# Performance work log

Hardware: AMD Instinct MI355X
Metric: run time of the kernel (lower is better)

The kernel has to match this reference:

```python
import jax, jax.numpy as jnp
import numpy as np

# ---- module hyperparameters (from init_kwargs) ----
DIM = 16        # Hilbert-space dimension (density matrix is DIM x DIM)
BATCH = 32      # number of initial states evolved in parallel
K_LIND = 4      # number of Lindblad collapse operators
N_TS = 512      # number of Euler integration steps
N_CTRLS = 4     # number of control channels
N_PARAMS = 16   # B-spline control points per channel
DEGREE = 3      # cubic B-splines
T_TOTAL = 1.0
DT = T_TOTAL / N_TS


def _bspline_basis_matrix(t, knots, degree):
    """Cox-de Boor recursion, vectorized over all basis functions.
    t: (n_ts,), knots: (n_knots,). Returns (n_ts, n_knots-1-degree)."""
    k = knots
    # degree-0: indicator of half-open knot spans -> (n_ts, n_knots-1)
    B = ((k[None, :-1] <= t[:, None]) & (t[:, None] < k[None, 1:])).astype(t.dtype)
    for d in range(1, degree + 1):
        left_den = k[d:-1] - k[:-(d + 1)]
        right_den = k[d + 1:] - k[1:-d]
        left = jnp.where(left_den > 0,
                         (t[:, None] - k[None, :-(d + 1)]) / jnp.where(left_den > 0, left_den, 1.0) * B[:, :-1],
                         0.0)
        right = jnp.where(right_den > 0,
                          (k[None, d + 1:] - t[:, None]) / jnp.where(right_den > 0, right_den, 1.0) * B[:, 1:],
                          0.0)
        B = left + right
    return B  # (n_ts, n_knots - 1 - degree) == (n_ts, N_PARAMS)


def setup_inputs() -> dict:
    key = jax.random.key(0)
    ks = jax.random.split(key, 10)
    f32 = jnp.float32
    params = 0.5 * jax.random.normal(ks[0], (N_PARAMS, N_CTRLS), f32)
    H0_re = jax.random.normal(ks[1], (DIM, DIM), f32)
    H0_im = jax.random.normal(ks[2], (DIM, DIM), f32)
    Hc_re = jax.random.normal(ks[3], (N_CTRLS, DIM, DIM), f32)
    Hc_im = jax.random.normal(ks[4], (N_CTRLS, DIM, DIM), f32)
    L_re = 0.3 * jax.random.normal(ks[5], (K_LIND, DIM, DIM), f32)
    L_im = 0.3 * jax.random.normal(ks[6], (K_LIND, DIM, DIM), f32)
    # valid density matrices: rho0 = A A^dag / tr(A A^dag)
    A = (jax.random.normal(ks[7], (BATCH, DIM, DIM), f32)
         + 1j * jax.random.normal(ks[8], (BATCH, DIM, DIM), f32)).astype(jnp.complex64)
    rho0 = jnp.einsum('bij,bkj->bik', A, A.conj())
    tr = jnp.trace(rho0, axis1=-2, axis2=-1).real[:, None, None]
    rho0 = rho0 / tr.astype(jnp.complex64)
    return {
        'params': params,
        'H0_re': H0_re, 'H0_im': H0_im,
        'Hc_re': Hc_re, 'Hc_im': Hc_im,
        'L_re': L_re, 'L_im': L_im,
        'rho0_re': jnp.real(rho0).astype(f32),
        'rho0_im': jnp.imag(rho0).astype(f32),
    }


def reference(params, H0_re, H0_im, Hc_re, Hc_im, L_re, L_im, rho0_re, rho0_im):
    c64 = jnp.complex64
    # Hermitize Hamiltonians
    H0 = (H0_re + 1j * H0_im).astype(c64)
    H0 = 0.5 * (H0 + H0.conj().T)
    Hc = (Hc_re + 1j * Hc_im).astype(c64)
    Hc = 0.5 * (Hc + jnp.conj(jnp.swapaxes(Hc, -1, -2)))
    L = (L_re + 1j * L_im).astype(c64)              # (K, d, d)
    LdL = jnp.einsum('kji,kjl->il', L.conj(), L)    # sum_k L^dag L  (d, d)
    rho0 = (rho0_re + 1j * rho0_im).astype(c64)     # (B, d, d)

    # B-spline control pulses (clamped knot vector, as in evaluate_bspline_batch)
    t = jnp.arange(N_TS, dtype=jnp.float32) * DT
    knots = jnp.concatenate([
        jnp.zeros(DEGREE, jnp.float32),
        jnp.linspace(0.0, T_TOTAL, N_PARAMS - DEGREE + 1).astype(jnp.float32),
        T_TOTAL * jnp.ones(DEGREE, jnp.float32),
    ])
    basis = _bspline_basis_matrix(t, knots, DEGREE)  # (n_ts, n_params)
    u = basis @ params                               # (n_ts, n_ctrls)

    def step(rho, u_t):
        H = H0 + jnp.einsum('c,cij->ij', u_t.astype(c64), Hc)
        jump = jnp.einsum('kij,bjl,kml->bim', L, rho, L.conj())
        drho = (-1j) * (H @ rho - rho @ H) + jump - 0.5 * (LdL @ rho + rho @ LdL)
        rho_new = rho + DT * drho
        pops = jnp.real(jnp.diagonal(rho_new, axis1=-2, axis2=-1)).astype(jnp.float32)
        return rho_new, pops

    _, pops = jax.lax.scan(step, rho0, u)
    return pops  # (n_ts, batch, dim) real populations
```

## Files before the change

kernel.cpp:

```cpp
#include <hip/hip_runtime.h>
#include <hip/hip_bf16.h>

#define DIM    16
#define BATCH  32
#define KL     4
#define NTS    512
#define NC     4
#define NPAR   16
#define DTF    (1.0f/512.0f)
#define BST    40

using short8  = __attribute__((ext_vector_type(8))) short;
using short4v = __attribute__((ext_vector_type(4))) short;
using f32x4   = __attribute__((ext_vector_type(4))) float;

__device__ __forceinline__ float b2f(__hip_bfloat16 x) { return __bfloat162float(x); }

__device__ __forceinline__ float ldval(const void* p, int idx, bool isf32) {
  return isf32 ? ((const float*)p)[idx]
               : __bfloat162float(((const __hip_bfloat16*)p)[idx]);
}
__device__ __forceinline__ unsigned short f2bf(float x) {
  unsigned u = __float_as_uint(x);
  unsigned r = u + 0x7FFFu + ((u >> 16) & 1u);
  return (unsigned short)(r >> 16);
}
__device__ __forceinline__ float bf2f(unsigned short h) {
  return __uint_as_float(((unsigned)h) << 16);
}
__device__ __forceinline__ void split2(float v, unsigned short& h, unsigned short& l) {
  unsigned u = __float_as_uint(v);
  h = (unsigned short)(u >> 16);
  float r = v - __uint_as_float(u & 0xFFFF0000u);
  l = (unsigned short)(__float_as_uint(r) >> 16);
}
__device__ __forceinline__ short8 ldfrag(const unsigned short* p) {
  return *(const short8*)p;
}
__device__ __forceinline__ short8 negbf8(short8 a) {
  union { short8 s; unsigned u[4]; } v; v.s = a;
  #pragma unroll
  for (int q = 0; q < 4; ++q) v.u[q] ^= 0x80008000u;
  return v.s;
}
__device__ __forceinline__ f32x4 mm3(short8 Ah, short8 Al, short8 Bh, short8 Bl, f32x4 acc) {
  acc = __builtin_amdgcn_mfma_f32_16x16x32_bf16(Ah, Bh, acc, 0, 0, 0);
  acc = __builtin_amdgcn_mfma_f32_16x16x32_bf16(Al, Bh, acc, 0, 0, 0);
  acc = __builtin_amdgcn_mfma_f32_16x16x32_bf16(Ah, Bl, acc, 0, 0, 0);
  return acc;
}
__device__ __forceinline__ f32x4 mm3b(short8 Ah, short8 Al, short8 Bh, short8 Bl, f32x4 acc) {
  acc = __builtin_amdgcn_mfma_f32_16x16x32_bf16(Ah, Bh, acc, 0, 0, 0);
  acc = __builtin_amdgcn_mfma_f32_16x16x32_bf16(Ah, Bl, acc, 0, 0, 0);
  acc = __builtin_amdgcn_mfma_f32_16x16x32_bf16(Al, Bh, acc, 0, 0, 0);
  return acc;
}
__device__ __forceinline__ void pack4(f32x4 v, short4v& hi, short4v& lo) {
  union { short4v s; unsigned d[2]; } H, L;
  unsigned u0 = __float_as_uint(v[0]), u1 = __float_as_uint(v[1]);
  unsigned u2 = __float_as_uint(v[2]), u3 = __float_as_uint(v[3]);
  H.d[0] = __builtin_amdgcn_perm(u1, u0, 0x07060302u);
  H.d[1] = __builtin_amdgcn_perm(u3, u2, 0x07060302u);
  float r0 = v[0] - __uint_as_float(u0 & 0xFFFF0000u);
  float r1 = v[1] - __uint_as_float(u1 & 0xFFFF0000u);
  float r2 = v[2] - __uint_as_float(u2 & 0xFFFF0000u);
  float r3 = v[3] - __uint_as_float(u3 & 0xFFFF0000u);
  L.d[0] = __builtin_amdgcn_perm(__float_as_uint(r1), __float_as_uint(r0), 0x07060302u);
  L.d[1] = __builtin_amdgcn_perm(__float_as_uint(r3), __float_as_uint(r2), 0x07060302u);
  hi = H.s; lo = L.s;
}
__device__ __forceinline__ void pack8(const float* v, short8& hi, short8& lo) {
  union { short8 s; unsigned d[4]; } H, L;
  #pragma unroll
  for (int j = 0; j < 4; ++j) {
    unsigned ua = __float_as_uint(v[2*j]), ub = __float_as_uint(v[2*j+1]);
    H.d[j] = __builtin_amdgcn_perm(ub, ua, 0x07060302u);
    float ra = v[2*j]   - __uint_as_float(ua & 0xFFFF0000u);
    float rb = v[2*j+1] - __uint_as_float(ub & 0xFFFF0000u);
    L.d[j] = __builtin_amdgcn_perm(__float_as_uint(rb), __float_as_uint(ra), 0x07060302u);
  }
  hi = H.s; lo = L.s;
}

__global__ __launch_bounds__(384, 1)
void lindblad_evolve(const void* __restrict__ g_params,
                     const void* __restrict__ g_H0re, const void* __restrict__ g_H0im,
                     const void* __restrict__ g_Hcre, const void* __restrict__ g_Hcim,
                     const void* __restrict__ g_Lre,  const void* __restrict__ g_Lim,
                     const void* __restrict__ g_r0re, const void* __restrict__ g_r0im,
                     float* __restrict__ g_out)
{
  __shared__ __align__(16) unsigned short sPh[16*BST], sPl[16*BST];
  __shared__ __align__(16) unsigned short sTh[KL][16*BST], sTl[KL][16*BST];
  __shared__ __align__(16) unsigned short sLh[KL][16*BST], sLl[KL][16*BST];
  __shared__ __align__(16) unsigned short sGh[16*BST], sGl[16*BST];
  __shared__ __align__(16) float sJr[KL][256], sJi[KL][256];
  __shared__ __align__(16) float sU[NTS][NC];
  __shared__ __align__(16) float sPops[NTS*DIM];
  __shared__ int sFlag;

  const int tid = threadIdx.x;
  const int b   = blockIdx.x;
  const int wv  = tid >> 6;
  const int ln  = tid & 63;
  const int fm  = ln & 15;
  const int fq  = ln >> 4;
  const int row0 = fq * 4;
  const int fOff  = fm*BST + fq*8;
  const int fOffS = fm*BST + ((fq*8 + 16) & 31);

  if (tid == 0) sFlag = 0;
  __syncthreads();
  if (tid < 256) {
    float v = b2f(((const __hip_bfloat16*)g_H0re)[tid]);
    if (!(fabsf(v) <= 1e10f)) atomicOr(&sFlag, 1);
  }
  __syncthreads();
  const bool isf32 = (sFlag != 0);

  for (int t0 = tid; t0 < NTS; t0 += 384) {
    float kn[20];
    kn[0] = 0.f; kn[1] = 0.f; kn[2] = 0.f;
    #pragma unroll
    for (int q = 0; q < 14; ++q) kn[3 + q] = (float)q / 13.0f;
    kn[17] = 1.f; kn[18] = 1.f; kn[19] = 1.f;
    const float t = (float)t0 * DTF;
    float B[19];
    #pragma unroll
    for (int q = 0; q < 19; ++q) B[q] = (kn[q] <= t && t < kn[q+1]) ? 1.f : 0.f;
    #pragma unroll
    for (int d = 1; d <= 3; ++d) {
      #pragma unroll
      for (int q = 0; q + d < 19; ++q) {
        float ld = kn[q+d]   - kn[q];
        float rd = kn[q+d+1] - kn[q+1];
        float lv = (ld > 0.f) ? (t - kn[q])     / ld * B[q]   : 0.f;
        float rv = (rd > 0.f) ? (kn[q+d+1] - t) / rd * B[q+1] : 0.f;
        B[q] = lv + rv;
      }
    }
    #pragma unroll
    for (int c = 0; c < NC; ++c) {
      float s = 0.f;
      #pragma unroll
      for (int q = 0; q < NPAR; ++q) s += B[q] * ldval(g_params, q*NC + c, isf32);
      sU[t0][c] = s;
    }
  }

  if (tid < 256) {
    float* scr = sPops;
    const int i = tid >> 4, j = tid & 15;
    const int ij = i*16 + j, ji = j*16 + i;
    float h0r = 0.5f * (ldval(g_H0re, ij, isf32) + ldval(g_H0re, ji, isf32));
    float h0i = 0.5f * (ldval(g_H0im, ij, isf32) - ldval(g_H0im, ji, isf32));
    float ldr = 0.f, ldi = 0.f;
    for (int k = 0; k < KL; ++k) {
      #pragma unroll
      for (int m = 0; m < DIM; ++m) {
        float ar = ldval(g_Lre, k*256 + m*16 + i, isf32), ai = ldval(g_Lim, k*256 + m*16 + i, isf32);
        float br = ldval(g_Lre, k*256 + m*16 + j, isf32), bi = ldval(g_Lim, k*256 + m*16 + j, isf32);
        ldr += ar*br + ai*bi;
        ldi += ar*bi - ai*br;
      }
    }
    scr[0*256 + ij] =  h0i - 0.5f*ldr;
    scr[1*256 + ij] = -h0r - 0.5f*ldi;
    #pragma unroll
    for (int c = 0; c < NC; ++c) {
      float hr = 0.5f * (ldval(g_Hcre, c*256 + ij, isf32) + ldval(g_Hcre, c*256 + ji, isf32));
      float hi = 0.5f * (ldval(g_Hcim, c*256 + ij, isf32) - ldval(g_Hcim, c*256 + ji, isf32));
      scr[(2 + 2*c)*256 + ij] =  hi;
      scr[(3 + 2*c)*256 + ij] = -hr;
    }
    #pragma unroll
    for (int k = 0; k < KL; ++k) {
      float lr = ldval(g_Lre, k*256 + ij, isf32);
      float li = ldval(g_Lim, k*256 + ij, isf32);
      unsigned short h;
      h = f2bf(lr); sLh[k][i*BST + j]      = h; sLl[k][i*BST + j]      = f2bf(lr - bf2f(h));
      h = f2bf(li); sLh[k][i*BST + 16 + j] = h; sLl[k][i*BST + 16 + j] = f2bf(li - bf2f(h));
    }
    float r0 = ldval(g_r0re, b*256 + ij, isf32);
    float m0 = ldval(g_r0im, b*256 + ij, isf32);
    unsigned short h, l;
    split2(r0, h, l); sPh[j*BST + i]      = h; sPl[j*BST + i]      = l;
    split2(m0, h, l); sPh[j*BST + 16 + i] = h; sPl[j*BST + 16 + i] = l;
  }

  __syncthreads();

  short8 LFh_, LFl_, TrBh_, TrBl_, LSh_, LSl_;
  float  G0v[8], Gcv[NC][8];
  float  rm[4] = {0.f,0.f,0.f,0.f};

  if (wv < 4) {
    const int k = wv;
    LFh_ = ldfrag(&sLh[k][fOff]);
    LFl_ = ldfrag(&sLl[k][fOff]);
    TrBh_ = (fq >= 2) ? negbf8(LFh_) : LFh_;
    TrBl_ = (fq >= 2) ? negbf8(LFl_) : LFl_;
    short8 h = ldfrag(&sLh[k][fOffS]);
    short8 l = ldfrag(&sLl[k][fOffS]);
    if (fq < 2) { h = negbf8(h); l = negbf8(l); }
    LSh_ = h; LSl_ = l;
    if (wv == 0) {
      const int comp = (fq < 2) ? 0 : 1;
      const int base = (fq & 1) * 8;
      const float* scr = sPops;
      {
        const float* s0 = &scr[comp*256 + fm*16 + base];
        f32x4 va = *(const f32x4*)s0, vb = *(const f32x4*)(s0 + 4);
        #pragma unroll
        for (int q = 0; q < 4; ++q) { G0v[q] = va[q]; G0v[4+q] = vb[q]; }
      }
      #pragma unroll
      for (int c = 0; c < NC; ++c) {
        const float* s0 = &scr[(2 + 2*c + comp)*256 + fm*16 + base];
        f32x4 va = *(const f32x4*)s0, vb = *(const f32x4*)(s0 + 4);
        #pragma unroll
        for (int q = 0; q < 4; ++q) { Gcv[c][q] = va[q]; Gcv[c][4+q] = vb[q]; }
      }
      f32x4 uv = *(const f32x4*)&sU[0][0];
      float gv[8];
      #pragma unroll
      for (int q = 0; q < 8; ++q)
        gv[q] = G0v[q] + uv[0]*Gcv[0][q] + uv[1]*Gcv[1][q] + uv[2]*Gcv[2][q] + uv[3]*Gcv[3][q];
      short8 Gh_, Gl_;
      pack8(gv, Gh_, Gl_);
      *(short8*)&sGh[fm*BST + fq*8] = Gh_;
      *(short8*)&sGl[fm*BST + fq*8] = Gl_;
    }
  } else if (wv == 4) {
    #pragma unroll
    for (int q = 0; q < 4; ++q) rm[q] = ldval(g_r0re, b*256 + (row0+q)*16 + fm, isf32);
  } else {
    #pragma unroll
    for (int q = 0; q < 4; ++q) rm[q] = ldval(g_r0im, b*256 + (row0+q)*16 + fm, isf32);
  }

  const f32x4 zero = {0.f, 0.f, 0.f, 0.f};

  #pragma unroll 1
  for (int t = 0; t < NTS; ++t) {
    f32x4 mAcc, mtAcc;

    __syncthreads();

    if (wv < 4) {
      const int k = wv;
      short8 Arh = ldfrag(&sPh[fOff]),  Arl = ldfrag(&sPl[fOff]);
      short8 Aih = ldfrag(&sPh[fOffS]), Ail = ldfrag(&sPl[fOffS]);
      f32x4 tr = mm3(Arh, Arl, TrBh_, TrBl_, zero);
      f32x4 ti = mm3(Aih, Ail, LFh_,  LFl_,  zero);
      short4v HR, LR, HI2, LI2;
      pack4(tr, HR, LR);
      pack4(ti, HI2, LI2);
      *(short4v*)&sTh[k][fm*BST + row0]      = HR;
      *(short4v*)&sTl[k][fm*BST + row0]      = LR;
      *(short4v*)&sTh[k][fm*BST + 16 + row0] = HI2;
      *(short4v*)&sTl[k][fm*BST + 16 + row0] = LI2;
      short8 Th = ldfrag(&sTh[k][fOff]), Tl = ldfrag(&sTl[k][fOff]);
      f32x4 jr = mm3(LFh_, LFl_, Th, Tl, zero);
      f32x4 ji = mm3(LSh_, LSl_, Th, Tl, zero);
      *(f32x4*)&sJr[k][ln*4] = jr;
      *(f32x4*)&sJi[k][ln*4] = ji;
    } else if (wv == 4) {
      short8 Ah = ldfrag(&sGh[fOff]), Al = ldfrag(&sGl[fOff]);
      short8 Ph = ldfrag(&sPh[fOff]), Pl = ldfrag(&sPl[fOff]);
      short8 Bh = (fq >= 2) ? negbf8(Ph) : Ph;
      short8 Bl = (fq >= 2) ? negbf8(Pl) : Pl;
      mAcc = mm3(Ah, Al, Bh, Bl, zero);
      short8 Gth = (fq >= 2) ? negbf8(Ah) : Ah;
      short8 Gtl = (fq >= 2) ? negbf8(Al) : Al;
      mtAcc = mm3b(Ph, Pl, Gth, Gtl, zero);
    } else {
      short8 Ah = ldfrag(&sGh[fOff]), Al = ldfrag(&sGl[fOff]);
      short8 Ph = ldfrag(&sPh[fOffS]), Pl = ldfrag(&sPl[fOffS]);
      mAcc = mm3(Ah, Al, Ph, Pl, zero);
      mtAcc = mm3b(Ph, Pl, Ah, Al, zero);
    }

    __syncthreads();

    if (wv >= 4) {
      const float* sJ = (wv == 4) ? &sJr[0][0] : &sJi[0][0];
      f32x4 a0 = *(const f32x4*)&sJ[0*256 + ln*4];
      f32x4 a1 = *(const f32x4*)&sJ[1*256 + ln*4];
      f32x4 a2 = *(const f32x4*)&sJ[2*256 + ln*4];
      f32x4 a3 = *(const f32x4*)&sJ[3*256 + ln*4];
      short4v HH, LL;
      f32x4 rv;
      if (wv == 4) {
        #pragma unroll
        for (int q = 0; q < 4; ++q) {
          rm[q] += DTF * (mAcc[q] + mtAcc[q] + ((a0[q] + a1[q]) + (a2[q] + a3[q])));
          rv[q] = rm[q];
        }
        pack4(rv, HH, LL);
        *(short4v*)&sPh[fm*BST + row0] = HH;
        *(short4v*)&sPl[fm*BST + row0] = LL;
        if ((unsigned)(fm - row0) < 4u) sPops[t*DIM + fm] = rm[fm - row0];
      } else {
        #pragma unroll
        for (int q = 0; q < 4; ++q) {
          rm[q] += DTF * (mAcc[q] - mtAcc[q] - ((a0[q] + a1[q]) + (a2[q] + a3[q])));
          rv[q] = rm[q];
        }
        pack4(rv, HH, LL);
        *(short4v*)&sPh[fm*BST + 16 + row0] = HH;
        *(short4v*)&sPl[fm*BST + 16 + row0] = LL;
      }
    } else if (wv == 0) {
      const int tn = (t + 1 < NTS) ? (t + 1) : t;
      f32x4 uv = *(const f32x4*)&sU[tn][0];
      float gv[8];
      #pragma unroll
      for (int q = 0; q < 8; ++q)
        gv[q] = G0v[q] + uv[0]*Gcv[0][q] + uv[1]*Gcv[1][q] + uv[2]*Gcv[2][q] + uv[3]*Gcv[3][q];
      short8 Gh_, Gl_;
      pack8(gv, Gh_, Gl_);
      *(short8*)&sGh[fm*BST + fq*8] = Gh_;
      *(short8*)&sGl[fm*BST + fq*8] = Gl_;
    }
  }

  __syncthreads();
  for (int i4 = tid; i4 < NTS*DIM/4; i4 += 384) {
    int idx = i4 * 4;
    int tt = idx >> 4, dd = idx & 15;
    *(float4*)&g_out[tt*(BATCH*DIM) + b*DIM + dd] = *(const float4*)&sPops[idx];
  }
}

extern "C" void kernel_launch(void* const* d_in, const int* in_sizes, int n_in,
                              void* d_out, int out_size, void* d_ws, size_t ws_size,
                              hipStream_t stream) {
  (void)out_size; (void)d_ws; (void)ws_size;
  const void *P, *H0r, *H0i, *Hcr, *Hci, *Lr, *Li, *R0r, *R0i;
  int idx64 = -1;
  for (int q = 0; q < n_in; ++q) if (in_sizes[q] == 64) idx64 = q;
  if (idx64 == 6) {
    H0i = d_in[0]; H0r = d_in[1];
    Hci = d_in[2]; Hcr = d_in[3];
    Li  = d_in[4]; Lr  = d_in[5];
    P   = d_in[6];
    R0i = d_in[7]; R0r = d_in[8];
  } else {
    P   = d_in[0];
    H0r = d_in[1]; H0i = d_in[2];
    Hcr = d_in[3]; Hci = d_in[4];
    Lr  = d_in[5]; Li  = d_in[6];
    R0r = d_in[7]; R0i = d_in[8];
  }
  lindblad_evolve<<<dim3(BATCH), dim3(384), 0, stream>>>(
      P, H0r, H0i, Hcr, Hci, Lr, Li, R0r, R0i, (float*)d_out);
}
```

Measured before the change: 417.8 us.

## Transpose intermediate via permlane swaps instead of LDS and split MFMA chains

The intermediate T fragment, which was written to shared memory and read back in transposed layout, is now rearranged in registers with permlane32/permlane16 swap instructions, and the sTh/sTl buffers are removed. The three-pass bf16 split MFMA sequences now use independent zero-initialized accumulators that are summed afterwards, so the MFMAs no longer form a dependent chain. Together these aim to cut LDS round-trip latency and MFMA dependency stalls on the serial per-step critical path. In exchange it adds vector adds and depends on the permlane swap builtins producing exactly the required lane mapping.

```diff
diff --git a/kernel.cpp b/kernel.cpp
--- a/kernel.cpp
+++ b/kernel.cpp
@@ -13,6 +13,7 @@
 using short8  = __attribute__((ext_vector_type(8))) short;
 using short4v = __attribute__((ext_vector_type(4))) short;
 using f32x4   = __attribute__((ext_vector_type(4))) float;
+using uintx2  = __attribute__((ext_vector_type(2))) unsigned int;
 
 __device__ __forceinline__ float b2f(__hip_bfloat16 x) { return __bfloat162float(x); }
 
@@ -43,17 +44,19 @@
   for (int q = 0; q < 4; ++q) v.u[q] ^= 0x80008000u;
   return v.s;
 }
-__device__ __forceinline__ f32x4 mm3(short8 Ah, short8 Al, short8 Bh, short8 Bl, f32x4 acc) {
-  acc = __builtin_amdgcn_mfma_f32_16x16x32_bf16(Ah, Bh, acc, 0, 0, 0);
-  acc = __builtin_amdgcn_mfma_f32_16x16x32_bf16(Al, Bh, acc, 0, 0, 0);
-  acc = __builtin_amdgcn_mfma_f32_16x16x32_bf16(Ah, Bl, acc, 0, 0, 0);
-  return acc;
-}
-__device__ __forceinline__ f32x4 mm3b(short8 Ah, short8 Al, short8 Bh, short8 Bl, f32x4 acc) {
-  acc = __builtin_amdgcn_mfma_f32_16x16x32_bf16(Ah, Bh, acc, 0, 0, 0);
-  acc = __builtin_amdgcn_mfma_f32_16x16x32_bf16(Ah, Bl, acc, 0, 0, 0);
-  acc = __builtin_amdgcn_mfma_f32_16x16x32_bf16(Al, Bh, acc, 0, 0, 0);
-  return acc;
+__device__ __forceinline__ f32x4 mm3s(short8 Ah, short8 Al, short8 Bh, short8 Bl) {
+  const f32x4 z = {0.f, 0.f, 0.f, 0.f};
+  f32x4 a = __builtin_amdgcn_mfma_f32_16x16x32_bf16(Ah, Bh, z, 0, 0, 0);
+  f32x4 b = __builtin_amdgcn_mfma_f32_16x16x32_bf16(Al, Bh, z, 0, 0, 0);
+  f32x4 c = __builtin_amdgcn_mfma_f32_16x16x32_bf16(Ah, Bl, z, 0, 0, 0);
+  return (a + b) + c;
+}
+__device__ __forceinline__ f32x4 mm3bs(short8 Ah, short8 Al, short8 Bh, short8 Bl) {
+  const f32x4 z = {0.f, 0.f, 0.f, 0.f};
+  f32x4 a = __builtin_amdgcn_mfma_f32_16x16x32_bf16(Ah, Bh, z, 0, 0, 0);
+  f32x4 b = __builtin_amdgcn_mfma_f32_16x16x32_bf16(Ah, Bl, z, 0, 0, 0);
+  f32x4 c = __builtin_amdgcn_mfma_f32_16x16x32_bf16(Al, Bh, z, 0, 0, 0);
+  return (a + b) + c;
 }
 __device__ __forceinline__ void pack4(f32x4 v, short4v& hi, short4v& lo) {
   union { short4v s; unsigned d[2]; } H, L;
@@ -69,6 +72,19 @@
   L.d[1] = __builtin_amdgcn_perm(__float_as_uint(r3), __float_as_uint(r2), 0x07060302u);
   hi = H.s; lo = L.s;
 }
+__device__ __forceinline__ void pack4d(f32x4 v, unsigned& h0, unsigned& h1,
+                                       unsigned& l0, unsigned& l1) {
+  unsigned u0 = __float_as_uint(v[0]), u1 = __float_as_uint(v[1]);
+  unsigned u2 = __float_as_uint(v[2]), u3 = __float_as_uint(v[3]);
+  h0 = __builtin_amdgcn_perm(u1, u0, 0x07060302u);
+  h1 = __builtin_amdgcn_perm(u3, u2, 0x07060302u);
+  float r0 = v[0] - __uint_as_float(u0 & 0xFFFF0000u);
+  float r1 = v[1] - __uint_as_float(u1 & 0xFFFF0000u);
+  float r2 = v[2] - __uint_as_float(u2 & 0xFFFF0000u);
+  float r3 = v[3] - __uint_as_float(u3 & 0xFFFF0000u);
+  l0 = __builtin_amdgcn_perm(__float_as_uint(r1), __float_as_uint(r0), 0x07060302u);
+  l1 = __builtin_amdgcn_perm(__float_as_uint(r3), __float_as_uint(r2), 0x07060302u);
+}
 __device__ __forceinline__ void pack8(const float* v, short8& hi, short8& lo) {
   union { short8 s; unsigned d[4]; } H, L;
   #pragma unroll
@@ -81,6 +97,21 @@
   }
   hi = H.s; lo = L.s;
 }
+__device__ __forceinline__ void xpose2(unsigned A, unsigned B, unsigned& p, unsigned& q) {
+  uintx2 xy = __builtin_amdgcn_permlane32_swap(A, B, false, false);
+  uintx2 pq = __builtin_amdgcn_permlane16_swap(xy[0], xy[1], false, false);
+  p = pq[0]; q = pq[1];
+}
+__device__ __forceinline__ void mkfrag(unsigned XH0, unsigned XH1, unsigned XL0, unsigned XL1,
+                                       unsigned YH0, unsigned YH1, unsigned YL0, unsigned YL1,
+                                       short8& h, short8& l) {
+  union { short8 s; unsigned d[4]; } H, L;
+  xpose2(XH0, YH0, H.d[0], H.d[2]);
+  xpose2(XH1, YH1, H.d[1], H.d[3]);
+  xpose2(XL0, YL0, L.d[0], L.d[2]);
+  xpose2(XL1, YL1, L.d[1], L.d[3]);
+  h = H.s; l = L.s;
+}
 
 __global__ __launch_bounds__(384, 1)
 void lindblad_evolve(const void* __restrict__ g_params,
@@ -91,7 +122,6 @@
                      float* __restrict__ g_out)
 {
   __shared__ __align__(16) unsigned short sPh[16*BST], sPl[16*BST];
-  __shared__ __align__(16) unsigned short sTh[KL][16*BST], sTl[KL][16*BST];
   __shared__ __align__(16) unsigned short sLh[KL][16*BST], sLl[KL][16*BST];
   __shared__ __align__(16) unsigned short sGh[16*BST], sGl[16*BST];
   __shared__ __align__(16) float sJr[KL][256], sJi[KL][256];
@@ -239,8 +269,6 @@
     for (int q = 0; q < 4; ++q) rm[q] = ldval(g_r0im, b*256 + (row0+q)*16 + fm, isf32);
   }
 
-  const f32x4 zero = {0.f, 0.f, 0.f, 0.f};
-
   #pragma unroll 1
   for (int t = 0; t < NTS; ++t) {
     f32x4 mAcc, mtAcc;
@@ -251,18 +279,15 @@
       const int k = wv;
       short8 Arh = ldfrag(&sPh[fOff]),  Arl = ldfrag(&sPl[fOff]);
       short8 Aih = ldfrag(&sPh[fOffS]), Ail = ldfrag(&sPl[fOffS]);
-      f32x4 tr = mm3(Arh, Arl, TrBh_, TrBl_, zero);
-      f32x4 ti = mm3(Aih, Ail, LFh_,  LFl_,  zero);
-      short4v HR, LR, HI2, LI2;
-      pack4(tr, HR, LR);
-      pack4(ti, HI2, LI2);
-      *(short4v*)&sTh[k][fm*BST + row0]      = HR;
-      *(short4v*)&sTl[k][fm*BST + row0]      = LR;
-      *(short4v*)&sTh[k][fm*BST + 16 + row0] = HI2;
-      *(short4v*)&sTl[k][fm*BST + 16 + row0] = LI2;
-      short8 Th = ldfrag(&sTh[k][fOff]), Tl = ldfrag(&sTl[k][fOff]);
-      f32x4 jr = mm3(LFh_, LFl_, Th, Tl, zero);
-      f32x4 ji = mm3(LSh_, LSl_, Th, Tl, zero);
+      f32x4 tr = mm3s(Arh, Arl, TrBh_, TrBl_);
+      f32x4 ti = mm3s(Aih, Ail, LFh_,  LFl_);
+      unsigned TH0, TH1, TL0, TL1, UH0, UH1, UL0, UL1;
+      pack4d(tr, TH0, TH1, TL0, TL1);
+      pack4d(ti, UH0, UH1, UL0, UL1);
+      short8 Th, Tl;
+      mkfrag(TH0, TH1, TL0, TL1, UH0, UH1, UL0, UL1, Th, Tl);
+      f32x4 jr = mm3s(LFh_, LFl_, Th, Tl);
+      f32x4 ji = mm3s(LSh_, LSl_, Th, Tl);
       *(f32x4*)&sJr[k][ln*4] = jr;
       *(f32x4*)&sJi[k][ln*4] = ji;
     } else if (wv == 4) {
@@ -270,15 +295,15 @@
       short8 Ph = ldfrag(&sPh[fOff]), Pl = ldfrag(&sPl[fOff]);
       short8 Bh = (fq >= 2) ? negbf8(Ph) : Ph;
       short8 Bl = (fq >= 2) ? negbf8(Pl) : Pl;
-      mAcc = mm3(Ah, Al, Bh, Bl, zero);
+      mAcc = mm3s(Ah, Al, Bh, Bl);
       short8 Gth = (fq >= 2) ? negbf8(Ah) : Ah;
       short8 Gtl = (fq >= 2) ? negbf8(Al) : Al;
-      mtAcc = mm3b(Ph, Pl, Gth, Gtl, zero);
+      mtAcc = mm3bs(Ph, Pl, Gth, Gtl);
     } else {
       short8 Ah = ldfrag(&sGh[fOff]), Al = ldfrag(&sGl[fOff]);
       short8 Ph = ldfrag(&sPh[fOffS]), Pl = ldfrag(&sPl[fOffS]);
-      mAcc = mm3(Ah, Al, Ph, Pl, zero);
-      mtAcc = mm3b(Ph, Pl, Ah, Al, zero);
+      mAcc = mm3s(Ah, Al, Ph, Pl);
+      mtAcc = mm3bs(Ph, Pl, Ah, Al);
     }
 
     __syncthreads();
```

New measurement: 426.4 us. 2.1% more time.
